# Kernel tuning notes

Hardware: AMD Instinct MI355X
Metric: run time of the kernel (lower is better)

The kernel has to match this reference:

```python
import jax, jax.numpy as jnp
import numpy as np

D_MODEL = 1024
D_HIDDEN = 4096
N_LATENTS = 64
D_LATENT = 1024
N_HEADS = 16
N_EXPERTS = 8
TOP_K = 2
B, T = 2, 2048
D_H = D_LATENT // N_HEADS  # 64


def setup_inputs() -> dict:
    key = jax.random.key(0)
    ks = jax.random.split(key, 16)
    x = jax.random.normal(ks[0], (B, T, D_MODEL), jnp.float32)
    # real RoPE cache (matches RoPE.build_rope_cache)
    half = D_H // 2
    inv_freq = 1.0 / (10000.0 ** (jnp.arange(half, dtype=jnp.float32) / half))
    ang = jnp.arange(T, dtype=jnp.float32)[:, None] * inv_freq[None, :]
    cos, sin = jnp.cos(ang), jnp.sin(ang)
    sL = D_LATENT ** -0.5
    sM = D_MODEL ** -0.5
    sH = D_HIDDEN ** -0.5
    def nrm(k, shape, sc):
        return jax.random.normal(k, shape, jnp.float32) * sc
    aks = jax.random.split(ks[1], 8)
    eks = jax.random.split(ks[2], 3)
    return {
        'x': x, 'cos': cos, 'sin': sin,
        'ln1_g': jnp.ones((D_MODEL,), jnp.float32), 'ln1_b': jnp.zeros((D_MODEL,), jnp.float32),
        'ln2_g': jnp.ones((D_MODEL,), jnp.float32), 'ln2_b': jnp.zeros((D_MODEL,), jnp.float32),
        'ln3_g': jnp.ones((D_MODEL,), jnp.float32), 'ln3_b': jnp.zeros((D_MODEL,), jnp.float32),
        'Lat': nrm(aks[0], (N_LATENTS, D_LATENT), sL),
        'Wq_lat': nrm(aks[1], (D_LATENT, D_LATENT), sL),
        'Wk_in': nrm(aks[2], (D_MODEL, D_LATENT), sM),
        'Wv_in': nrm(aks[3], (D_MODEL, D_LATENT), sM),
        'Wq_in': nrm(aks[4], (D_MODEL, D_LATENT), sM),
        'Wk_lat': nrm(aks[5], (D_LATENT, D_LATENT), sL),
        'Wv_lat': nrm(aks[6], (D_LATENT, D_LATENT), sL),
        'Wout_attn': nrm(aks[7], (D_LATENT, D_MODEL), sL),
        'router_W': nrm(ks[3], (D_MODEL, N_EXPERTS), sM),
        'router_b': jnp.zeros((N_EXPERTS,), jnp.float32),
        'expert_W': nrm(eks[0], (N_EXPERTS, D_MODEL, D_HIDDEN), sM),
        'expert_V': nrm(eks[1], (N_EXPERTS, D_MODEL, D_HIDDEN), sM),
        'expert_Wo': nrm(eks[2], (N_EXPERTS, D_HIDDEN, D_MODEL), sH),
        'lin_W': nrm(ks[4], (D_MODEL, D_MODEL), sM),
        'lin_b': jnp.zeros((D_MODEL,), jnp.float32),
    }


def _layernorm(x, g, b):
    mean = jnp.mean(x, axis=-1, keepdims=True)
    std = jnp.std(x, axis=-1, keepdims=True, ddof=1)  # torch std is unbiased
    return g * (x - mean) / (std + 1e-06) + b


def _split_heads(x):
    b, t, _ = x.shape
    return x.reshape(b, t, N_HEADS, D_H).transpose(0, 2, 1, 3)  # [b,h,t,dh]


def _merge_heads(x):
    b, h, t, dh = x.shape
    return x.transpose(0, 2, 1, 3).reshape(b, t, h * dh)


def _apply_rope(x, cos, sin):
    b, h, s, d = x.shape
    xr = x.reshape(b, h, s, d // 2, 2)
    x1, x2 = xr[..., 0], xr[..., 1]
    c = cos[:s][None, None]
    sn = sin[:s][None, None]
    o1 = x1 * c - x2 * sn
    o2 = x1 * sn + x2 * c
    return jnp.stack([o1, o2], axis=-1).reshape(b, h, s, d)


def _attn(Q, K, V):
    scores = jnp.einsum('bhqd,bhkd->bhqk', Q, K) / (D_H ** 0.5)
    w = jax.nn.softmax(scores, axis=-1)
    return jnp.einsum('bhqk,bhkd->bhqd', w, V)


def _mlha(x, cos, sin, Lat, Wq_lat, Wk_in, Wv_in, Wq_in, Wk_lat, Wv_lat, Wout_attn):
    b = x.shape[0]
    Lb = jnp.broadcast_to(Lat[None], (b, N_LATENTS, D_LATENT))
    Q = _split_heads(Lb @ Wq_lat)
    K = _apply_rope(_split_heads(x @ Wk_in), cos, sin)
    V = _split_heads(x @ Wv_in)
    z = _merge_heads(_attn(Q, K, V))              # [b, n_latents, d_latent]
    Ql = _split_heads(z @ Wq_lat)
    Kl = _split_heads(z @ Wk_lat)
    Vl = _split_heads(z @ Wv_lat)
    z2 = _merge_heads(_attn(Ql, Kl, Vl))          # [b, n_latents, d_latent]
    Qx = _apply_rope(_split_heads(x @ Wq_in), cos, sin)
    Kz = _split_heads(z2 @ Wk_lat)
    Vz = _split_heads(z2 @ Wv_lat)
    xl = _merge_heads(_attn(Qx, Kz, Vz))          # [b, T, d_latent]
    return xl @ Wout_attn


def _moe(x, router_W, router_b, expert_W, expert_V, expert_Wo):
    b, t, d = x.shape
    xf = x.reshape(b * t, d)
    logits = xf @ router_W + router_b                       # [N, E]
    topv, topi = jax.lax.top_k(logits, TOP_K)               # [N, k]
    probs = jax.nn.softmax(topv, axis=-1)                   # [N, k]
    out = jnp.zeros_like(xf)
    for e in range(N_EXPERTS):
        gate = jnp.sum(jnp.where(topi == e, probs, 0.0), axis=-1)  # [N]
        a = xf @ expert_W[e]
        bb = xf @ expert_V[e]
        y = (a * (bb * jax.nn.sigmoid(bb))) @ expert_Wo[e]
        out = out + gate[:, None] * y
    return out.reshape(b, t, d)


def reference(x, cos, sin, ln1_g, ln1_b, ln2_g, ln2_b, ln3_g, ln3_b,
              Lat, Wq_lat, Wk_in, Wv_in, Wq_in, Wk_lat, Wv_lat, Wout_attn,
              router_W, router_b, expert_W, expert_V, expert_Wo, lin_W, lin_b):
    attn = _mlha(x, cos, sin, Lat, Wq_lat, Wk_in, Wv_in, Wq_in, Wk_lat, Wv_lat, Wout_attn)
    x = _layernorm(x, ln1_g, ln1_b) + attn
    x = _layernorm(x, ln2_g, ln2_b) + _moe(x, router_W, router_b, expert_W, expert_V, expert_Wo)
    x = _layernorm(x, ln3_g, ln3_b) + (x @ lin_W + lin_b)
    return x
```

## Files before the change

### kernel.cpp

```cpp
#include <hip/hip_runtime.h>
#include <hip/hip_bf16.h>
#include <math.h>

typedef __hip_bfloat16 bf16;
typedef __attribute__((ext_vector_type(8))) short short8;
typedef __attribute__((ext_vector_type(8))) unsigned short ushort8;
typedef __attribute__((ext_vector_type(4))) float f32x4;

#define NT_   2048
#define NTOK_ 4096
#define DM_   1024
#define DHID_ 4096
#define NEXP_ 8

__device__ __forceinline__ unsigned short f2bf(float f) {
    unsigned u = __float_as_uint(f);
    u = u + 0x7FFF + ((u >> 16) & 1);
    return (unsigned short)(u >> 16);
}

__global__ __launch_bounds__(256) void c2b(const float* __restrict__ in,
        unsigned short* __restrict__ out, int n8)
{
    int i = blockIdx.x * 256 + threadIdx.x;
    if (i >= n8) return;
    const float4 v0 = *(const float4*)(in + (size_t)i * 8);
    const float4 v1 = *(const float4*)(in + (size_t)i * 8 + 4);
    ushort8 o;
    o[0] = f2bf(v0.x); o[1] = f2bf(v0.y); o[2] = f2bf(v0.z); o[3] = f2bf(v0.w);
    o[4] = f2bf(v1.x); o[5] = f2bf(v1.y); o[6] = f2bf(v1.z); o[7] = f2bf(v1.w);
    *(ushort8*)(out + (size_t)i * 8) = o;
}

__global__ __launch_bounds__(256) void tconv(const float* __restrict__ in,
        unsigned short* __restrict__ out, int R, int C)
{
    __shared__ float t[64][65];
    const size_t mofs = (size_t)blockIdx.z * R * C;
    const int r0 = blockIdx.y * 64, c0 = blockIdx.x * 64;
    const int tid = threadIdx.x;
    const int lr = tid >> 4, lc4 = (tid & 15) * 4;
    #pragma unroll
    for (int i = 0; i < 4; ++i) {
        float4 v = *(const float4*)(in + mofs + (size_t)(r0 + lr + i * 16) * C + c0 + lc4);
        t[lr + i * 16][lc4 + 0] = v.x; t[lr + i * 16][lc4 + 1] = v.y;
        t[lr + i * 16][lc4 + 2] = v.z; t[lr + i * 16][lc4 + 3] = v.w;
    }
    __syncthreads();
    const int oc = tid >> 2;
    const int j0 = (tid & 3) * 16;
    ushort8 o0, o1;
    #pragma unroll
    for (int j = 0; j < 8; ++j)  o0[j] = f2bf(t[j0 + j][oc]);
    #pragma unroll
    for (int j = 0; j < 8; ++j)  o1[j] = f2bf(t[j0 + 8 + j][oc]);
    size_t ob = mofs + (size_t)(c0 + oc) * R + r0 + j0;
    *(ushort8*)(out + ob) = o0;
    *(ushort8*)(out + ob + 8) = o1;
}

__global__ __launch_bounds__(256) void tconv3(const float* __restrict__ s0,
        const float* __restrict__ s1, const float* __restrict__ s2,
        unsigned short* __restrict__ out)
{
    __shared__ float t[64][65];
    const float* in = blockIdx.z == 0 ? s0 : (blockIdx.z == 1 ? s1 : s2);
    unsigned short* o = out + (size_t)blockIdx.z * DM_ * DM_;
    const int r0 = blockIdx.y * 64, c0 = blockIdx.x * 64;
    const int tid = threadIdx.x;
    const int lr = tid >> 4, lc4 = (tid & 15) * 4;
    #pragma unroll
    for (int i = 0; i < 4; ++i) {
        float4 v = *(const float4*)(in + (size_t)(r0 + lr + i * 16) * DM_ + c0 + lc4);
        t[lr + i * 16][lc4 + 0] = v.x; t[lr + i * 16][lc4 + 1] = v.y;
        t[lr + i * 16][lc4 + 2] = v.z; t[lr + i * 16][lc4 + 3] = v.w;
    }
    __syncthreads();
    const int oc = tid >> 2;
    const int j0 = (tid & 3) * 16;
    ushort8 o0, o1;
    #pragma unroll
    for (int j = 0; j < 8; ++j)  o0[j] = f2bf(t[j0 + j][oc]);
    #pragma unroll
    for (int j = 0; j < 8; ++j)  o1[j] = f2bf(t[j0 + 8 + j][oc]);
    size_t ob = (size_t)(c0 + oc) * DM_ + r0 + j0;
    *(ushort8*)(o + ob) = o0;
    *(ushort8*)(o + ob + 8) = o1;
}

__global__ __launch_bounds__(256) void gemm_bf16_128(
        const unsigned short* __restrict__ A, const unsigned short* __restrict__ BT,
        float* __restrict__ C, int M, int N, int K)
{
    __shared__ unsigned short As[128 * 64];
    __shared__ unsigned short Bs[128 * 64];
    const int tid = threadIdx.x;
    const int wid = tid >> 6, lane = tid & 63;
    const int m0 = blockIdx.y * 128, n0 = blockIdx.x * 128;

    const unsigned short* aSrc[4]; const unsigned short* bSrc[4]; int sWr[4];
    #pragma unroll
    for (int i = 0; i < 4; ++i) {
        int idx = tid + 256 * i;
        int row = idx >> 3, c8 = idx & 7;
        int ar = m0 + row; if (ar >= M) ar = M - 1;
        aSrc[i] = A + (size_t)ar * K + c8 * 8;
        bSrc[i] = BT + (size_t)(n0 + row) * K + c8 * 8;
        sWr[i] = (row * 128 + c8 * 16) ^ ((row & 7) << 4);
    }
    const int wr = wid >> 1, wc = wid & 1;
    int ra[2][4], rb[2][4];
    #pragma unroll
    for (int kk = 0; kk < 2; ++kk) {
        #pragma unroll
        for (int t = 0; t < 4; ++t) {
            int kb = kk * 64 + (lane >> 4) * 16;
            int rowa = wr * 64 + t * 16 + (lane & 15);
            ra[kk][t] = (rowa * 128 + kb) ^ ((rowa & 7) << 4);
            int rowb = wc * 64 + t * 16 + (lane & 15);
            rb[kk][t] = (rowb * 128 + kb) ^ ((rowb & 7) << 4);
        }
    }
    const f32x4 zero = {0.f, 0.f, 0.f, 0.f};
    f32x4 acc[4][4];
    #pragma unroll
    for (int i = 0; i < 4; ++i)
        #pragma unroll
        for (int j = 0; j < 4; ++j) acc[i][j] = zero;

    short8 sa[4], sb[4];
    #pragma unroll
    for (int i = 0; i < 4; ++i) { sa[i] = *(const short8*)(aSrc[i]); sb[i] = *(const short8*)(bSrc[i]); }
    const int nk = K >> 6;
    for (int kt = 0; kt < nk; ++kt) {
        #pragma unroll
        for (int i = 0; i < 4; ++i) {
            *(short8*)((char*)As + sWr[i]) = sa[i];
            *(short8*)((char*)Bs + sWr[i]) = sb[i];
        }
        __syncthreads();
        if (kt + 1 < nk) {
            int ko = (kt + 1) << 6;
            #pragma unroll
            for (int i = 0; i < 4; ++i) { sa[i] = *(const short8*)(aSrc[i] + ko); sb[i] = *(const short8*)(bSrc[i] + ko); }
        }
        #pragma unroll
        for (int kk = 0; kk < 2; ++kk) {
            short8 af[4], bfr[4];
            #pragma unroll
            for (int t = 0; t < 4; ++t) {
                af[t]  = *(const short8*)((const char*)As + ra[kk][t]);
                bfr[t] = *(const short8*)((const char*)Bs + rb[kk][t]);
            }
            #pragma unroll
            for (int i = 0; i < 4; ++i)
                #pragma unroll
                for (int j = 0; j < 4; ++j)
                    acc[i][j] = __builtin_amdgcn_mfma_f32_16x16x32_bf16(af[i], bfr[j], acc[i][j], 0, 0, 0);
        }
        __syncthreads();
    }
    const int cl = lane & 15, g4 = lane >> 4;
    #pragma unroll
    for (int i = 0; i < 4; ++i)
        #pragma unroll
        for (int j = 0; j < 4; ++j)
            #pragma unroll
            for (int r = 0; r < 4; ++r) {
                int rr = m0 + wr * 64 + i * 16 + g4 * 4 + r;
                if (rr < M) C[(size_t)rr * N + n0 + wc * 64 + j * 16 + cl] = acc[i][j][r];
            }
}

__global__ __launch_bounds__(256) void gemm_proj3(
        const unsigned short* __restrict__ A, const unsigned short* __restrict__ BT0,
        float* __restrict__ C0, const float* __restrict__ cosb,
        const float* __restrict__ sinb)
{
    const int z = blockIdx.z;
    const unsigned short* BT = BT0 + (size_t)z * DM_ * DM_;
    float* C = C0 + (size_t)z * NTOK_ * DM_;
    const bool doRope = (z != 1);
    __shared__ unsigned short As[128 * 64];
    __shared__ unsigned short Bs[128 * 64];
    const int tid = threadIdx.x;
    const int wid = tid >> 6, lane = tid & 63;
    const int m0 = blockIdx.y * 128, n0 = blockIdx.x * 128;
    const int K = DM_, N = DM_;

    const unsigned short* aSrc[4]; const unsigned short* bSrc[4]; int sWr[4];
    #pragma unroll
    for (int i = 0; i < 4; ++i) {
        int idx = tid + 256 * i;
        int row = idx >> 3, c8 = idx & 7;
        aSrc[i] = A + (size_t)(m0 + row) * K + c8 * 8;
        bSrc[i] = BT + (size_t)(n0 + row) * K + c8 * 8;
        sWr[i] = (row * 128 + c8 * 16) ^ ((row & 7) << 4);
    }
    const int wr = wid >> 1, wc = wid & 1;
    int ra[2][4], rb[2][4];
    #pragma unroll
    for (int kk = 0; kk < 2; ++kk) {
        #pragma unroll
        for (int t = 0; t < 4; ++t) {
            int kb = kk * 64 + (lane >> 4) * 16;
            int rowa = wr * 64 + t * 16 + (lane & 15);
            ra[kk][t] = (rowa * 128 + kb) ^ ((rowa & 7) << 4);
            int rowb = wc * 64 + t * 16 + (lane & 15);
            rb[kk][t] = (rowb * 128 + kb) ^ ((rowb & 7) << 4);
        }
    }
    const f32x4 zero = {0.f, 0.f, 0.f, 0.f};
    f32x4 acc[4][4];
    #pragma unroll
    for (int i = 0; i < 4; ++i)
        #pragma unroll
        for (int j = 0; j < 4; ++j) acc[i][j] = zero;

    short8 sa[4], sb[4];
    #pragma unroll
    for (int i = 0; i < 4; ++i) { sa[i] = *(const short8*)(aSrc[i]); sb[i] = *(const short8*)(bSrc[i]); }
    const int nk = K >> 6;
    for (int kt = 0; kt < nk; ++kt) {
        #pragma unroll
        for (int i = 0; i < 4; ++i) {
            *(short8*)((char*)As + sWr[i]) = sa[i];
            *(short8*)((char*)Bs + sWr[i]) = sb[i];
        }
        __syncthreads();
        if (kt + 1 < nk) {
            int ko = (kt + 1) << 6;
            #pragma unroll
            for (int i = 0; i < 4; ++i) { sa[i] = *(const short8*)(aSrc[i] + ko); sb[i] = *(const short8*)(bSrc[i] + ko); }
        }
        #pragma unroll
        for (int kk = 0; kk < 2; ++kk) {
            short8 af[4], bfr[4];
            #pragma unroll
            for (int t = 0; t < 4; ++t) {
                af[t]  = *(const short8*)((const char*)As + ra[kk][t]);
                bfr[t] = *(const short8*)((const char*)Bs + rb[kk][t]);
            }
            #pragma unroll
            for (int i = 0; i < 4; ++i)
                #pragma unroll
                for (int j = 0; j < 4; ++j)
                    acc[i][j] = __builtin_amdgcn_mfma_f32_16x16x32_bf16(af[i], bfr[j], acc[i][j], 0, 0, 0);
        }
        __syncthreads();
    }
    const int cl = lane & 15, g4 = lane >> 4;
    #pragma unroll
    for (int i = 0; i < 4; ++i)
        #pragma unroll
        for (int j = 0; j < 4; ++j) {
            const int cc = n0 + wc * 64 + j * 16 + cl;
            const int ii = (cc & 63) >> 1;
            const bool even = (cc & 1) == 0;
            #pragma unroll
            for (int r = 0; r < 4; ++r) {
                const int rr = m0 + wr * 64 + i * 16 + g4 * 4 + r;
                float v = acc[i][j][r];
                float p = __shfl_xor(v, 1, 64);
                float o = v;
                if (doRope) {
                    const int t = rr & (NT_ - 1);
                    float cv = cosb[t * 32 + ii], sv = sinb[t * 32 + ii];
                    o = even ? (v * cv - p * sv) : (p * sv + v * cv);
                }
                C[(size_t)rr * N + cc] = o;
            }
        }
}

__global__ __launch_bounds__(256) void gemm_lat(
        const unsigned short* __restrict__ A, const unsigned short* __restrict__ BT0,
        int btStride, float* __restrict__ C0, int cStride, int M)
{
    const int z = blockIdx.y;
    const unsigned short* BT = BT0 + (size_t)z * btStride;
    float* C = C0 + (size_t)z * cStride;
    const int n0 = blockIdx.x * 64;
    __shared__ unsigned short As[128 * 64];
    __shared__ unsigned short Bs[64 * 64];
    const int tid = threadIdx.x;
    const int wid = tid >> 6, lane = tid & 63;

    const unsigned short* aSrc[4]; int aWr[4];
    #pragma unroll
    for (int i = 0; i < 4; ++i) {
        int idx = tid + 256 * i;
        int row = idx >> 3, c8 = idx & 7;
        int ar = row; if (ar >= M) ar = M - 1;
        aSrc[i] = A + (size_t)ar * DM_ + c8 * 8;
        aWr[i] = (row * 128 + c8 * 16) ^ ((row & 7) << 4);
    }
    const unsigned short* bSrc[2]; int bWr[2];
    #pragma unroll
    for (int i = 0; i < 2; ++i) {
        int idx = tid + 256 * i;
        int row = idx >> 3, c8 = idx & 7;
        bSrc[i] = BT + (size_t)(n0 + row) * DM_ + c8 * 8;
        bWr[i] = (row * 128 + c8 * 16) ^ ((row & 7) << 4);
    }
    const int wr = wid >> 1, wc = wid & 1;
    int ra[2][4], rb[2][2];
    #pragma unroll
    for (int kk = 0; kk < 2; ++kk) {
        #pragma unroll
        for (int t = 0; t < 4; ++t) {
            int rowa = wr * 64 + t * 16 + (lane & 15);
            int kb = kk * 64 + (lane >> 4) * 16;
            ra[kk][t] = (rowa * 128 + kb) ^ ((rowa & 7) << 4);
        }
        #pragma unroll
        for (int t = 0; t < 2; ++t) {
            int rowb = wc * 32 + t * 16 + (lane & 15);
            int kb = kk * 64 + (lane >> 4) * 16;
            rb[kk][t] = (rowb * 128 + kb) ^ ((rowb & 7) << 4);
        }
    }
    const f32x4 zero = {0.f, 0.f, 0.f, 0.f};
    f32x4 acc[4][2];
    #pragma unroll
    for (int i = 0; i < 4; ++i)
        #pragma unroll
        for (int j = 0; j < 2; ++j) acc[i][j] = zero;

    short8 sa[4], sb[2];
    #pragma unroll
    for (int i = 0; i < 4; ++i) sa[i] = *(const short8*)(aSrc[i]);
    #pragma unroll
    for (int i = 0; i < 2; ++i) sb[i] = *(const short8*)(bSrc[i]);
    const int nk = DM_ >> 6;
    for (int kt = 0; kt < nk; ++kt) {
        #pragma unroll
        for (int i = 0; i < 4; ++i) *(short8*)((char*)As + aWr[i]) = sa[i];
        #pragma unroll
        for (int i = 0; i < 2; ++i) *(short8*)((char*)Bs + bWr[i]) = sb[i];
        __syncthreads();
        if (kt + 1 < nk) {
            int ko = (kt + 1) << 6;
            #pragma unroll
            for (int i = 0; i < 4; ++i) sa[i] = *(const short8*)(aSrc[i] + ko);
            #pragma unroll
            for (int i = 0; i < 2; ++i) sb[i] = *(const short8*)(bSrc[i] + ko);
        }
        #pragma unroll
        for (int kk = 0; kk < 2; ++kk) {
            short8 af[4], bf2[2];
            #pragma unroll
            for (int t = 0; t < 4; ++t) af[t] = *(const short8*)((const char*)As + ra[kk][t]);
            #pragma unroll
            for (int t = 0; t < 2; ++t) bf2[t] = *(const short8*)((const char*)Bs + rb[kk][t]);
            #pragma unroll
            for (int i = 0; i < 4; ++i)
                #pragma unroll
                for (int j = 0; j < 2; ++j)
                    acc[i][j] = __builtin_amdgcn_mfma_f32_16x16x32_bf16(af[i], bf2[j], acc[i][j], 0, 0, 0);
        }
        __syncthreads();
    }
    const int cl = lane & 15, g4 = lane >> 4;
    #pragma unroll
    for (int i = 0; i < 4; ++i)
        #pragma unroll
        for (int j = 0; j < 2; ++j)
            #pragma unroll
            for (int r = 0; r < 4; ++r) {
                int rl = wr * 64 + i * 16 + g4 * 4 + r;
                if (rl < M)
                    C[(size_t)rl * DM_ + n0 + wc * 32 + j * 16 + cl] = acc[i][j][r];
            }
}

__global__ __launch_bounds__(256) void attn_scores(float* __restrict__ S,
        const float* __restrict__ Q, const float* __restrict__ Km,
        int M, int T, int q_bs, int k_bs, float scale)
{
    const int bh = blockIdx.z, b = bh >> 4, h = bh & 15;
    const int t0 = blockIdx.x * 64, q0 = blockIdx.y * 64;
    __shared__ float Qs[64][65], Ks[64][65];
    const int tid = threadIdx.x;
    const int lr = tid >> 2, lc = (tid & 3) * 16;
    {
        int q = q0 + lr;
        if (q < M) {
            const float* Qp = Q + ((size_t)q_bs * b + q) * DM_ + h * 64 + lc;
            #pragma unroll
            for (int j = 0; j < 16; ++j) Qs[lr][lc + j] = Qp[j];
        } else {
            #pragma unroll
            for (int j = 0; j < 16; ++j) Qs[lr][lc + j] = 0.f;
        }
        const float* Kp = Km + ((size_t)k_bs * b + t0 + lr) * DM_ + h * 64 + lc;
        #pragma unroll
        for (int j = 0; j < 16; ++j) Ks[lr][lc + j] = Kp[j];
    }
    __syncthreads();
    const int ty = tid >> 4, tx = tid & 15;
    float acc[4][4] = {};
    for (int d = 0; d < 64; ++d) {
        float a[4], kk[4];
        #pragma unroll
        for (int i = 0; i < 4; ++i) a[i] = Qs[ty * 4 + i][d];
        #pragma unroll
        for (int j = 0; j < 4; ++j) kk[j] = Ks[tx * 4 + j][d];
        #pragma unroll
        for (int i = 0; i < 4; ++i)
            #pragma unroll
            for (int j = 0; j < 4; ++j) acc[i][j] += a[i] * kk[j];
    }
    #pragma unroll
    for (int i = 0; i < 4; ++i) {
        int q = q0 + ty * 4 + i;
        if (q < M) {
            float* Sp = S + ((size_t)bh * M + q) * T + t0 + tx * 4;
            #pragma unroll
            for (int j = 0; j < 4; ++j) Sp[j] = acc[i][j] * scale;
        }
    }
}

__global__ __launch_bounds__(256) void softmax_rows(float* __restrict__ S, int L)
{
    float* p = S + (size_t)blockIdx.x * L;
    const int tid = threadIdx.x;
    __shared__ float red[256];
    float m = -1e30f;
    for (int i = tid; i < L; i += 256) m = fmaxf(m, p[i]);
    red[tid] = m; __syncthreads();
    for (int s = 128; s; s >>= 1) { if (tid < s) red[tid] = fmaxf(red[tid], red[tid + s]); __syncthreads(); }
    m = red[0]; __syncthreads();
    float sum = 0.f;
    for (int i = tid; i < L; i += 256) { float e = __expf(p[i] - m); p[i] = e; sum += e; }
    red[tid] = sum; __syncthreads();
    for (int s = 128; s; s >>= 1) { if (tid < s) red[tid] += red[tid + s]; __syncthreads(); }
    float inv = 1.f / red[0];
    for (int i = tid; i < L; i += 256) p[i] *= inv;
}

__global__ __launch_bounds__(256) void softmax64(float* __restrict__ S)
{
    const int row = blockIdx.x * 4 + (threadIdx.x >> 6);
    const int lane = threadIdx.x & 63;
    float* p = S + (size_t)row * 64;
    float v = p[lane];
    float m = v;
    #pragma unroll
    for (int o = 32; o; o >>= 1) m = fmaxf(m, __shfl_xor(m, o, 64));
    float e = __expf(v - m);
    float s = e;
    #pragma unroll
    for (int o = 32; o; o >>= 1) s += __shfl_xor(s, o, 64);
    p[lane] = e / s;
}

__global__ __launch_bounds__(256) void pv_split(float* __restrict__ part,
        const float* __restrict__ P, const float* __restrict__ V)
{
    const int c = blockIdx.x, bh = blockIdx.y, b = bh >> 4, h = bh & 15;
    __shared__ float Ps[64][65], Vs[64][65];
    const int tid = threadIdx.x;
    const int lr = tid >> 2, lc = (tid & 3) * 16;
    const int ty = tid >> 4, tx = tid & 15;
    float acc[4][4] = {};
    for (int it = 0; it < 4; ++it) {
        const int t0 = c * 256 + it * 64;
        const float* Pp = P + ((size_t)bh * 64 + lr) * NT_ + t0 + lc;
        #pragma unroll
        for (int j = 0; j < 16; ++j) Ps[lr][lc + j] = Pp[j];
        const float* Vp = V + ((size_t)NT_ * b + t0 + lr) * DM_ + h * 64 + lc;
        #pragma unroll
        for (int j = 0; j < 16; ++j) Vs[lr][lc + j] = Vp[j];
        __syncthreads();
        for (int t = 0; t < 64; ++t) {
            float pp[4], vv[4];
            #pragma unroll
            for (int i = 0; i < 4; ++i) pp[i] = Ps[ty * 4 + i][t];
            #pragma unroll
            for (int j = 0; j < 4; ++j) vv[j] = Vs[t][tx * 4 + j];
            #pragma unroll
            for (int i = 0; i < 4; ++i)
                #pragma unroll
                for (int j = 0; j < 4; ++j) acc[i][j] += pp[i] * vv[j];
        }
        __syncthreads();
    }
    float* op = part + ((size_t)bh * 8 + c) * 4096;
    #pragma unroll
    for (int i = 0; i < 4; ++i)
        #pragma unroll
        for (int j = 0; j < 4; ++j)
            op[(ty * 4 + i) * 64 + tx * 4 + j] = acc[i][j];
}

__global__ __launch_bounds__(256) void pv_combine(const float* __restrict__ part,
        unsigned short* __restrict__ Zb)
{
    const int bh = blockIdx.x, b = bh >> 4, h = bh & 15;
    for (int idx = threadIdx.x; idx < 4096; idx += 256) {
        int q = idx >> 6, d = idx & 63;
        float s = 0.f;
        #pragma unroll
        for (int c = 0; c < 8; ++c) s += part[((size_t)bh * 8 + c) * 4096 + idx];
        Zb[(size_t)(b * 64 + q) * DM_ + h * 64 + d] = f2bf(s);
    }
}

__global__ __launch_bounds__(256) void attn_pv(float* __restrict__ Z,
        unsigned short* __restrict__ Zb,
        const float* __restrict__ P, const float* __restrict__ V,
        int M, int T, int v_bs)
{
    const int bh = blockIdx.y, b = bh >> 4, h = bh & 15;
    const int q0 = blockIdx.x * 64;
    __shared__ float Ps[64][65], Vs[64][65];
    const int tid = threadIdx.x;
    const int lr = tid >> 2, lc = (tid & 3) * 16;
    const int ty = tid >> 4, tx = tid & 15;
    float acc[4][4] = {};
    for (int t0 = 0; t0 < T; t0 += 64) {
        int q = q0 + lr;
        if (q < M) {
            const float* Pp = P + ((size_t)bh * M + q) * T + t0 + lc;
            #pragma unroll
            for (int j = 0; j < 16; ++j) Ps[lr][lc + j] = Pp[j];
        } else {
            #pragma unroll
            for (int j = 0; j < 16; ++j) Ps[lr][lc + j] = 0.f;
        }
        const float* Vp = V + ((size_t)v_bs * b + t0 + lr) * DM_ + h * 64 + lc;
        #pragma unroll
        for (int j = 0; j < 16; ++j) Vs[lr][lc + j] = Vp[j];
        __syncthreads();
        for (int t = 0; t < 64; ++t) {
            float pp[4], vv[4];
            #pragma unroll
            for (int i = 0; i < 4; ++i) pp[i] = Ps[ty * 4 + i][t];
            #pragma unroll
            for (int j = 0; j < 4; ++j) vv[j] = Vs[t][tx * 4 + j];
            #pragma unroll
            for (int i = 0; i < 4; ++i)
                #pragma unroll
                for (int j = 0; j < 4; ++j) acc[i][j] += pp[i] * vv[j];
        }
        __syncthreads();
    }
    #pragma unroll
    for (int i = 0; i < 4; ++i) {
        int q = q0 + ty * 4 + i;
        if (q < M) {
            size_t ofs = ((size_t)b * M + q) * DM_ + h * 64 + tx * 4;
            #pragma unroll
            for (int j = 0; j < 4; ++j) {
                Z[ofs + j] = acc[i][j];
                Zb[ofs + j] = f2bf(acc[i][j]);
            }
        }
    }
}

__global__ __launch_bounds__(256) void ln_add_dual(const float* __restrict__ X,
        const float* __restrict__ g, const float* __restrict__ bb,
        const float* __restrict__ add, float* __restrict__ out,
        unsigned short* __restrict__ outb)
{
    const int n = blockIdx.x, tid = threadIdx.x;
    const float* x = X + (size_t)n * DM_;
    __shared__ float red[256];
    float v[4]; float s = 0.f;
    #pragma unroll
    for (int i = 0; i < 4; ++i) { v[i] = x[tid + i * 256]; s += v[i]; }
    red[tid] = s; __syncthreads();
    for (int st = 128; st; st >>= 1) { if (tid < st) red[tid] += red[tid + st]; __syncthreads(); }
    float mean = red[0] * (1.f / 1024.f);
    __syncthreads();
    float vs = 0.f;
    #pragma unroll
    for (int i = 0; i < 4; ++i) { float d = v[i] - mean; vs += d * d; }
    red[tid] = vs; __syncthreads();
    for (int st = 128; st; st >>= 1) { if (tid < st) red[tid] += red[tid + st]; __syncthreads(); }
    float inv = 1.f / (sqrtf(red[0] * (1.f / 1023.f)) + 1e-6f);
    #pragma unroll
    for (int i = 0; i < 4; ++i) {
        int d = tid + i * 256;
        float r = g[d] * (v[i] - mean) * inv + bb[d] + add[(size_t)n * DM_ + d];
        out[(size_t)n * DM_ + d] = r;
        outb[(size_t)n * DM_ + d] = f2bf(r);
    }
}

__global__ __launch_bounds__(256) void ln_final(const float* __restrict__ X,
        const float* __restrict__ g, const float* __restrict__ bb,
        const float* __restrict__ t, const float* __restrict__ lb,
        float* __restrict__ out)
{
    const int n = blockIdx.x, tid = threadIdx.x;
    const float* x = X + (size_t)n * DM_;
    __shared__ float red[256];
    float v[4]; float s = 0.f;
    #pragma unroll
    for (int i = 0; i < 4; ++i) { v[i] = x[tid + i * 256]; s += v[i]; }
    red[tid] = s; __syncthreads();
    for (int st = 128; st; st >>= 1) { if (tid < st) red[tid] += red[tid + st]; __syncthreads(); }
    float mean = red[0] * (1.f / 1024.f);
    __syncthreads();
    float vs = 0.f;
    #pragma unroll
    for (int i = 0; i < 4; ++i) { float d = v[i] - mean; vs += d * d; }
    red[tid] = vs; __syncthreads();
    for (int st = 128; st; st >>= 1) { if (tid < st) red[tid] += red[tid + st]; __syncthreads(); }
    float inv = 1.f / (sqrtf(red[0] * (1.f / 1023.f)) + 1e-6f);
    #pragma unroll
    for (int i = 0; i < 4; ++i) {
        int d = tid + i * 256;
        out[(size_t)n * DM_ + d] = g[d] * (v[i] - mean) * inv + bb[d]
                                 + t[(size_t)n * DM_ + d] + lb[d];
    }
}

__global__ __launch_bounds__(256) void router_kernel(const float* __restrict__ X1,
        const float* __restrict__ Wr, const float* __restrict__ br,
        int* __restrict__ topi, float* __restrict__ gates, int* __restrict__ counts)
{
    const int n = blockIdx.x, tid = threadIdx.x;
    const int e = tid >> 5, l = tid & 31;
    const float* x = X1 + (size_t)n * DM_;
    float s = 0.f;
    for (int k = l; k < DM_; k += 32) s += x[k] * Wr[k * NEXP_ + e];
    for (int off = 16; off; off >>= 1) s += __shfl_down(s, off, 32);
    __shared__ float lg[NEXP_];
    if (l == 0) lg[e] = s + br[e];
    __syncthreads();
    if (tid == 0) {
        float v1 = -1e30f; int i1 = 0;
        for (int ee = 0; ee < NEXP_; ++ee) if (lg[ee] > v1) { v1 = lg[ee]; i1 = ee; }
        float v2 = -1e30f; int i2 = 0;
        for (int ee = 0; ee < NEXP_; ++ee) if (ee != i1 && lg[ee] > v2) { v2 = lg[ee]; i2 = ee; }
        float e2 = __expf(v2 - v1);
        float inv = 1.f / (1.f + e2);
        topi[n * 2] = i1; topi[n * 2 + 1] = i2;
        gates[n * 2] = inv; gates[n * 2 + 1] = e2 * inv;
        atomicAdd(&counts[i1], 1); atomicAdd(&counts[i2], 1);
    }
}

__global__ void zero_counts(int* __restrict__ counts)
{
    if (threadIdx.x < NEXP_) counts[threadIdx.x] = 0;
}

__global__ void router_offsets(const int* __restrict__ counts, int* __restrict__ offs,
                               int* __restrict__ fill)
{
    if (threadIdx.x == 0) {
        int acc = 0;
        for (int e = 0; e < NEXP_; ++e) { offs[e] = acc; acc += counts[e]; fill[e] = 0; }
    }
}

__global__ __launch_bounds__(256) void router_scatter(const int* __restrict__ topi,
        int* __restrict__ fill, const int* __restrict__ offs,
        int* __restrict__ ptok, int* __restrict__ pidx)
{
    int n = blockIdx.x * 256 + threadIdx.x;
    if (n >= NTOK_) return;
    #pragma unroll
    for (int s2 = 0; s2 < 2; ++s2) {
        int e = topi[n * 2 + s2];
        int r = atomicAdd(&fill[e], 1);
        int p = offs[e] + r;
        ptok[p] = n;
        pidx[n * 2 + s2] = p;
    }
}

__global__ __launch_bounds__(256) void moe_up_mfma(
        const unsigned short* __restrict__ X1b,
        const unsigned short* __restrict__ WTa, const unsigned short* __restrict__ VTa,
        unsigned short* __restrict__ H,
        const int* __restrict__ cnt, const int* __restrict__ offs,
        const int* __restrict__ ptok)
{
    const int e = blockIdx.z;
    const int ce = cnt[e];
    const int m0 = blockIdx.y * 128;
    if (m0 >= ce) return;
    const int n0 = blockIdx.x * 64;
    const int base = offs[e];
    const unsigned short* WT = WTa + (size_t)e * DHID_ * DM_;
    const unsigned short* VT = VTa + (size_t)e * DHID_ * DM_;
    __shared__ unsigned short As[128 * 64];
    __shared__ unsigned short Ws[64 * 64];
    __shared__ unsigned short Vs[64 * 64];
    __shared__ int rtok[128];
    const int tid = threadIdx.x;
    const int wid = tid >> 6, lane = tid & 63;
    if (tid < 128) {
        int r = m0 + tid;
        rtok[tid] = (r < ce) ? ptok[base + r] : ptok[base + ce - 1];
    }
    __syncthreads();

    const unsigned short* aSrc[4]; int aWr[4];
    #pragma unroll
    for (int i = 0; i < 4; ++i) {
        int idx = tid + 256 * i;
        int row = idx >> 3, c8 = idx & 7;
        aSrc[i] = X1b + (size_t)rtok[row] * DM_ + c8 * 8;
        aWr[i] = (row * 128 + c8 * 16) ^ ((row & 7) << 4);
    }
    const unsigned short* wSrc[2]; const unsigned short* vSrc[2]; int bWr[2];
    #pragma unroll
    for (int i = 0; i < 2; ++i) {
        int idx = tid + 256 * i;
        int row = idx >> 3, c8 = idx & 7;
        wSrc[i] = WT + (size_t)(n0 + row) * DM_ + c8 * 8;
        vSrc[i] = VT + (size_t)(n0 + row) * DM_ + c8 * 8;
        bWr[i] = (row * 128 + c8 * 16) ^ ((row & 7) << 4);
    }
    const int wr = wid >> 1, wc = wid & 1;
    int ra[2][4], rb[2][2];
    #pragma unroll
    for (int kk = 0; kk < 2; ++kk) {
        #pragma unroll
        for (int t = 0; t < 4; ++t) {
            int rowa = wr * 64 + t * 16 + (lane & 15);
            int kb = kk * 64 + (lane >> 4) * 16;
            ra[kk][t] = (rowa * 128 + kb) ^ ((rowa & 7) << 4);
        }
        #pragma unroll
        for (int t = 0; t < 2; ++t) {
            int rowb = wc * 32 + t * 16 + (lane & 15);
            int kb = kk * 64 + (lane >> 4) * 16;
            rb[kk][t] = (rowb * 128 + kb) ^ ((rowb & 7) << 4);
        }
    }
    const f32x4 zero = {0.f, 0.f, 0.f, 0.f};
    f32x4 accw[4][2], accv[4][2];
    #pragma unroll
    for (int i = 0; i < 4; ++i)
        #pragma unroll
        for (int j = 0; j < 2; ++j) { accw[i][j] = zero; accv[i][j] = zero; }

    short8 sa[4], sw[2], sv[2];
    #pragma unroll
    for (int i = 0; i < 4; ++i) sa[i] = *(const short8*)(aSrc[i]);
    #pragma unroll
    for (int i = 0; i < 2; ++i) { sw[i] = *(const short8*)(wSrc[i]); sv[i] = *(const short8*)(vSrc[i]); }
    const int nk = DM_ >> 6;
    for (int kt = 0; kt < nk; ++kt) {
        #pragma unroll
        for (int i = 0; i < 4; ++i) *(short8*)((char*)As + aWr[i]) = sa[i];
        #pragma unroll
        for (int i = 0; i < 2; ++i) {
            *(short8*)((char*)Ws + bWr[i]) = sw[i];
            *(short8*)((char*)Vs + bWr[i]) = sv[i];
        }
        __syncthreads();
        if (kt + 1 < nk) {
            int ko = (kt + 1) << 6;
            #pragma unroll
            for (int i = 0; i < 4; ++i) sa[i] = *(const short8*)(aSrc[i] + ko);
            #pragma unroll
            for (int i = 0; i < 2; ++i) { sw[i] = *(const short8*)(wSrc[i] + ko); sv[i] = *(const short8*)(vSrc[i] + ko); }
        }
        #pragma unroll
        for (int kk = 0; kk < 2; ++kk) {
            short8 af[4], bw[2], bv[2];
            #pragma unroll
            for (int t = 0; t < 4; ++t) af[t] = *(const short8*)((const char*)As + ra[kk][t]);
            #pragma unroll
            for (int t = 0; t < 2; ++t) {
                bw[t] = *(const short8*)((const char*)Ws + rb[kk][t]);
                bv[t] = *(const short8*)((const char*)Vs + rb[kk][t]);
            }
            #pragma unroll
            for (int i = 0; i < 4; ++i)
                #pragma unroll
                for (int j = 0; j < 2; ++j) {
                    accw[i][j] = __builtin_amdgcn_mfma_f32_16x16x32_bf16(af[i], bw[j], accw[i][j], 0, 0, 0);
                    accv[i][j] = __builtin_amdgcn_mfma_f32_16x16x32_bf16(af[i], bv[j], accv[i][j], 0, 0, 0);
                }
        }
        __syncthreads();
    }
    const int cl = lane & 15, g4 = lane >> 4;
    #pragma unroll
    for (int i = 0; i < 4; ++i)
        #pragma unroll
        for (int j = 0; j < 2; ++j)
            #pragma unroll
            for (int r = 0; r < 4; ++r) {
                int rl = m0 + wr * 64 + i * 16 + g4 * 4 + r;
                if (rl < ce) {
                    float a = accw[i][j][r], b = accv[i][j][r];
                    float h = a * (b / (1.f + __expf(-b)));
                    H[(size_t)(base + rl) * DHID_ + n0 + wc * 32 + j * 16 + cl] = f2bf(h);
                }
            }
}

__global__ __launch_bounds__(256) void moe_down_mfma(
        const unsigned short* __restrict__ H, const unsigned short* __restrict__ WoTa,
        float* __restrict__ PY,
        const int* __restrict__ cnt, const int* __restrict__ offs)
{
    const int e = blockIdx.z;
    const int ce = cnt[e];
    const int m0 = blockIdx.y * 128;
    if (m0 >= ce) return;
    const int n0 = blockIdx.x * 128;
    const int base = offs[e];
    const unsigned short* WoT = WoTa + (size_t)e * DM_ * DHID_;
    __shared__ unsigned short As[128 * 64];
    __shared__ unsigned short Bs[128 * 64];
    const int tid = threadIdx.x;
    const int wid = tid >> 6, lane = tid & 63;

    const unsigned short* aSrc[4]; const unsigned short* bSrc[4]; int sWr[4];
    #pragma unroll
    for (int i = 0; i < 4; ++i) {
        int idx = tid + 256 * i;
        int row = idx >> 3, c8 = idx & 7;
        int r = m0 + row; if (r >= ce) r = ce - 1;
        aSrc[i] = H + (size_t)(base + r) * DHID_ + c8 * 8;
        bSrc[i] = WoT + (size_t)(n0 + row) * DHID_ + c8 * 8;
        sWr[i] = (row * 128 + c8 * 16) ^ ((row & 7) << 4);
    }
    const int wr = wid >> 1, wc = wid & 1;
    int ra[2][4], rb[2][4];
    #pragma unroll
    for (int kk = 0; kk < 2; ++kk) {
        #pragma unroll
        for (int t = 0; t < 4; ++t) {
            int kb = kk * 64 + (lane >> 4) * 16;
            int rowa = wr * 64 + t * 16 + (lane & 15);
            ra[kk][t] = (rowa * 128 + kb) ^ ((rowa & 7) << 4);
            int rowb = wc * 64 + t * 16 + (lane & 15);
            rb[kk][t] = (rowb * 128 + kb) ^ ((rowb & 7) << 4);
        }
    }
    const f32x4 zero = {0.f, 0.f, 0.f, 0.f};
    f32x4 acc[4][4];
    #pragma unroll
    for (int i = 0; i < 4; ++i)
        #pragma unroll
        for (int j = 0; j < 4; ++j) acc[i][j] = zero;

    short8 sa[4], sb[4];
    #pragma unroll
    for (int i = 0; i < 4; ++i) { sa[i] = *(const short8*)(aSrc[i]); sb[i] = *(const short8*)(bSrc[i]); }
    const int nk = DHID_ >> 6;
    for (int kt = 0; kt < nk; ++kt) {
        #pragma unroll
        for (int i = 0; i < 4; ++i) {
            *(short8*)((char*)As + sWr[i]) = sa[i];
            *(short8*)((char*)Bs + sWr[i]) = sb[i];
        }
        __syncthreads();
        if (kt + 1 < nk) {
            int ko = (kt + 1) << 6;
            #pragma unroll
            for (int i = 0; i < 4; ++i) { sa[i] = *(const short8*)(aSrc[i] + ko); sb[i] = *(const short8*)(bSrc[i] + ko); }
        }
        #pragma unroll
        for (int kk = 0; kk < 2; ++kk) {
            short8 af[4], bfr[4];
            #pragma unroll
            for (int t = 0; t < 4; ++t) {
                af[t]  = *(const short8*)((const char*)As + ra[kk][t]);
                bfr[t] = *(const short8*)((const char*)Bs + rb[kk][t]);
            }
            #pragma unroll
            for (int i = 0; i < 4; ++i)
                #pragma unroll
                for (int j = 0; j < 4; ++j)
                    acc[i][j] = __builtin_amdgcn_mfma_f32_16x16x32_bf16(af[i], bfr[j], acc[i][j], 0, 0, 0);
        }
        __syncthreads();
    }
    const int cl = lane & 15, g4 = lane >> 4;
    #pragma unroll
    for (int i = 0; i < 4; ++i)
        #pragma unroll
        for (int j = 0; j < 4; ++j)
            #pragma unroll
            for (int r = 0; r < 4; ++r) {
                int rl = m0 + wr * 64 + i * 16 + g4 * 4 + r;
                if (rl < ce)
                    PY[(size_t)(base + rl) * DM_ + n0 + wc * 64 + j * 16 + cl] = acc[i][j][r];
            }
}

__global__ __launch_bounds__(256) void moe_combine(const float* __restrict__ PY,
        const int* __restrict__ pidx, const float* __restrict__ gates,
        float* __restrict__ MO)
{
    int n = blockIdx.x, tid = threadIdx.x;
    int p0 = pidx[n * 2], p1 = pidx[n * 2 + 1];
    float g0 = gates[n * 2], g1 = gates[n * 2 + 1];
    #pragma unroll
    for (int i = 0; i < 4; ++i) {
        int d = tid + i * 256;
        MO[(size_t)n * DM_ + d] = g0 * PY[(size_t)p0 * DM_ + d] + g1 * PY[(size_t)p1 * DM_ + d];
    }
}

extern "C" void kernel_launch(void* const* d_in, const int* in_sizes, int n_in,
                              void* d_out, int out_size, void* d_ws, size_t ws_size,
                              hipStream_t stream)
{
    const float* x      = (const float*)d_in[0];
    const float* cosb   = (const float*)d_in[1];
    const float* sinb   = (const float*)d_in[2];
    const float* ln1g   = (const float*)d_in[3];
    const float* ln1b   = (const float*)d_in[4];
    const float* ln2g   = (const float*)d_in[5];
    const float* ln2b   = (const float*)d_in[6];
    const float* ln3g   = (const float*)d_in[7];
    const float* ln3b   = (const float*)d_in[8];
    const float* Lat    = (const float*)d_in[9];
    const float* Wq_lat = (const float*)d_in[10];
    const float* Wk_in  = (const float*)d_in[11];
    const float* Wv_in  = (const float*)d_in[12];
    const float* Wq_in  = (const float*)d_in[13];
    const float* Wk_lat = (const float*)d_in[14];
    const float* Wv_lat = (const float*)d_in[15];
    const float* Wout   = (const float*)d_in[16];
    const float* rW     = (const float*)d_in[17];
    const float* rb     = (const float*)d_in[18];
    const float* eW     = (const float*)d_in[19];
    const float* eV     = (const float*)d_in[20];
    const float* eWo    = (const float*)d_in[21];
    const float* linW   = (const float*)d_in[22];
    const float* linb   = (const float*)d_in[23];
    float* out = (float*)d_out;

    float* ws = (float*)d_ws;
    const size_t M1 = 1024 * 1024;
    float* buf0 = ws;
    float* buf1 = ws + 4 * M1;
    float* buf2 = ws + 8 * M1;
    float* buf3 = ws + 12 * M1;
    size_t off = 16 * M1;
    float* qlat = ws + off; off += 65536;
    float* qlb  = ws + off; off += 131072;
    float* klb  = ws + off; off += 131072;
    float* vlb  = ws + off; off += 131072;
    float* s2b  = ws + off; off += 131072;
    float* z2b  = ws + off; off += 131072;
    float* kzb  = ws + off; off += 131072;
    float* vzb  = ws + off; off += 131072;
    float* gates = ws + off; off += 8192;
    int* iarea = (int*)(ws + off); off += 32768;
    int* topi   = iarea;
    int* counts = iarea + 8192;
    int* offs   = iarea + 8200;
    int* fill   = iarea + 8208;
    int* ptok   = iarea + 8216;
    int* pidx   = iarea + 16408;
    unsigned short* zb_b  = (unsigned short*)(ws + off); off += 65536;
    unsigned short* z2b_b = (unsigned short*)(ws + off); off += 65536;
    unsigned short* latb  = (unsigned short*)(ws + off); off += 32768;
    unsigned short* x1b   = (unsigned short*)(ws + off); off += 2 * M1;
    unsigned short* WkT   = (unsigned short*)(ws + off); off += 3 * (M1 / 2);
    unsigned short* WoutT = (unsigned short*)(ws + off); off += M1 / 2;
    unsigned short* linWT = (unsigned short*)(ws + off); off += M1 / 2;
    unsigned short* WlatT = (unsigned short*)(ws + off); off += 3 * (M1 / 2);

    unsigned short* Hbuf  = (unsigned short*)(ws + 24 * M1);
    unsigned short* actb  = (unsigned short*)(ws + 24 * M1);
    unsigned short* x2b   = (unsigned short*)(ws + 24 * M1);
    float* pvpart         = ws + 26 * M1;
    unsigned short* eWT   = (unsigned short*)(ws + 40 * M1);
    unsigned short* eVT   = (unsigned short*)(ws + 56 * M1);
    unsigned short* eWoT  = eWT;
    float* PY             = ws + 56 * M1;

    dim3 blk(256);

    zero_counts<<<1, 64, 0, stream>>>(counts);

    tconv3<<<dim3(16, 16, 3), blk, 0, stream>>>(Wk_in, Wv_in, Wq_in, WkT);
    tconv<<<dim3(16, 16, 1), blk, 0, stream>>>(Wout, WoutT, 1024, 1024);
    tconv<<<dim3(16, 16, 1), blk, 0, stream>>>(linW, linWT, 1024, 1024);
    tconv3<<<dim3(16, 16, 3), blk, 0, stream>>>(Wq_lat, Wk_lat, Wv_lat, WlatT);
    tconv<<<dim3(64, 16, 8), blk, 0, stream>>>(eW, eWT, 1024, 4096);
    tconv<<<dim3(64, 16, 8), blk, 0, stream>>>(eV, eVT, 1024, 4096);
    c2b<<<2048, blk, 0, stream>>>(x, actb, 524288);
    c2b<<<32, blk, 0, stream>>>(Lat, latb, 8192);

    gemm_lat<<<dim3(16, 1), blk, 0, stream>>>(latb, WlatT, (int)M1, qlat, 0, 64);

    gemm_proj3<<<dim3(8, 32, 3), blk, 0, stream>>>(actb, WkT, buf0, cosb, sinb);

    attn_scores<<<dim3(32, 1, 32), blk, 0, stream>>>(buf3, qlat, buf0, 64, 2048, 0, 2048, 0.125f);
    softmax_rows<<<2048, blk, 0, stream>>>(buf3, 2048);
    pv_split<<<dim3(8, 32), blk, 0, stream>>>(pvpart, buf3, buf1);
    pv_combine<<<32, blk, 0, stream>>>(pvpart, zb_b);

    gemm_lat<<<dim3(16, 3), blk, 0, stream>>>(zb_b, WlatT, (int)M1, qlb, 131072, 128);
    attn_scores<<<dim3(1, 1, 32), blk, 0, stream>>>(s2b, qlb, klb, 64, 64, 64, 64, 0.125f);
    softmax64<<<512, blk, 0, stream>>>(s2b);
    attn_pv<<<dim3(1, 32), blk, 0, stream>>>(z2b, z2b_b, s2b, vlb, 64, 64, 64);

    gemm_lat<<<dim3(16, 2), blk, 0, stream>>>(z2b_b, WlatT + M1, (int)M1, kzb, 131072, 128);
    attn_scores<<<dim3(1, 32, 32), blk, 0, stream>>>(buf3, buf2, kzb, 2048, 64, 2048, 64, 0.125f);
    softmax64<<<16384, blk, 0, stream>>>(buf3);
    attn_pv<<<dim3(32, 32), blk, 0, stream>>>(buf0, actb, buf3, vzb, 2048, 64, 64);
    gemm_bf16_128<<<dim3(8, 32), blk, 0, stream>>>(actb, WoutT, buf1, 4096, 1024, 1024);

    ln_add_dual<<<4096, blk, 0, stream>>>(x, ln1g, ln1b, buf1, buf2, x1b);

    router_kernel<<<4096, blk, 0, stream>>>(buf2, rW, rb, topi, gates, counts);
    router_offsets<<<1, 64, 0, stream>>>(counts, offs, fill);
    router_scatter<<<16, blk, 0, stream>>>(topi, fill, offs, ptok, pidx);
    moe_up_mfma<<<dim3(64, 32, 8), blk, 0, stream>>>(x1b, eWT, eVT, Hbuf, counts, offs, ptok);
    tconv<<<dim3(16, 64, 8), blk, 0, stream>>>(eWo, eWoT, 4096, 1024);
    moe_down_mfma<<<dim3(8, 32, 8), blk, 0, stream>>>(Hbuf, eWoT, PY, counts, offs);
    moe_combine<<<4096, blk, 0, stream>>>(PY, pidx, gates, buf0);

    ln_add_dual<<<4096, blk, 0, stream>>>(buf2, ln2g, ln2b, buf0, buf1, x2b);

    gemm_bf16_128<<<dim3(8, 32), blk, 0, stream>>>(x2b, linWT, buf3, 4096, 1024, 1024);
    ln_final<<<4096, blk, 0, stream>>>(buf1, ln3g, ln3b, buf3, linb, out);
}
```

Baseline: 1.022 ms.

## Fuse 64-key attention scores, softmax and PV into one kernel

Replaces the three-kernel sequence (attn_scores, softmax64, attn_pv) for the two attention stages with 64 keys with a single fused kernel. The kernel keeps Q, K and V tiles in shared memory, computes scores, applies softmax with in-register shuffles and multiplies by V without writing the score matrix to global memory. This removes the round trip of a 4096x64 fp32 score matrix per head and two kernel launches per stage. It also drops the fp32 Z output and writes only bf16, and it uses about 50KB of shared memory per block, which may limit occupancy.

```diff
diff --git a/kernel.cpp b/kernel.cpp
--- a/kernel.cpp
+++ b/kernel.cpp
@@ -440,20 +440,81 @@
     for (int i = tid; i < L; i += 256) p[i] *= inv;
 }
 
-__global__ __launch_bounds__(256) void softmax64(float* __restrict__ S)
-{
-    const int row = blockIdx.x * 4 + (threadIdx.x >> 6);
-    const int lane = threadIdx.x & 63;
-    float* p = S + (size_t)row * 64;
-    float v = p[lane];
-    float m = v;
-    #pragma unroll
-    for (int o = 32; o; o >>= 1) m = fmaxf(m, __shfl_xor(m, o, 64));
-    float e = __expf(v - m);
-    float s = e;
-    #pragma unroll
-    for (int o = 32; o; o >>= 1) s += __shfl_xor(s, o, 64);
-    p[lane] = e / s;
+__global__ __launch_bounds__(256) void fused_attn64(unsigned short* __restrict__ Ob,
+        const float* __restrict__ Q, const float* __restrict__ Kp,
+        const float* __restrict__ Vp, int q_bs)
+{
+    const int bh = blockIdx.y, b = bh >> 4, h = bh & 15;
+    const int q0 = blockIdx.x * 64;
+    __shared__ float Qs[64][65], Ks[64][65], Vs[64][65];
+    __shared__ float ls[64];
+    const int tid = threadIdx.x;
+    const int lr = tid >> 2, lc = (tid & 3) * 16;
+    {
+        const float* Qr = Q + ((size_t)q_bs * b + q0 + lr) * DM_ + h * 64 + lc;
+        #pragma unroll
+        for (int j = 0; j < 16; ++j) Qs[lr][lc + j] = Qr[j];
+        const float* Kr = Kp + ((size_t)64 * b + lr) * DM_ + h * 64 + lc;
+        #pragma unroll
+        for (int j = 0; j < 16; ++j) Ks[lr][lc + j] = Kr[j];
+        const float* Vr = Vp + ((size_t)64 * b + lr) * DM_ + h * 64 + lc;
+        #pragma unroll
+        for (int j = 0; j < 16; ++j) Vs[lr][lc + j] = Vr[j];
+    }
+    __syncthreads();
+    const int ty = tid >> 4, tx = tid & 15;
+    float acc[4][4] = {};
+    for (int d = 0; d < 64; ++d) {
+        float a[4], kk[4];
+        #pragma unroll
+        for (int i = 0; i < 4; ++i) a[i] = Qs[ty * 4 + i][d];
+        #pragma unroll
+        for (int j = 0; j < 4; ++j) kk[j] = Ks[tx * 4 + j][d];
+        #pragma unroll
+        for (int i = 0; i < 4; ++i)
+            #pragma unroll
+            for (int j = 0; j < 4; ++j) acc[i][j] += a[i] * kk[j];
+    }
+    float p[4][4]; float lsum[4];
+    #pragma unroll
+    for (int i = 0; i < 4; ++i) {
+        float m = fmaxf(fmaxf(acc[i][0], acc[i][1]), fmaxf(acc[i][2], acc[i][3]));
+        #pragma unroll
+        for (int o = 1; o <= 8; o <<= 1) m = fmaxf(m, __shfl_xor(m, o, 64));
+        float s = 0.f;
+        #pragma unroll
+        for (int j = 0; j < 4; ++j) { p[i][j] = __expf(acc[i][j] * 0.125f - m * 0.125f); s += p[i][j]; }
+        #pragma unroll
+        for (int o = 1; o <= 8; o <<= 1) s += __shfl_xor(s, o, 64);
+        lsum[i] = s;
+    }
+    __syncthreads();
+    #pragma unroll
+    for (int i = 0; i < 4; ++i) {
+        #pragma unroll
+        for (int j = 0; j < 4; ++j) Qs[ty * 4 + i][tx * 4 + j] = p[i][j];
+        if (tx == 0) ls[ty * 4 + i] = lsum[i];
+    }
+    __syncthreads();
+    float O[4][4] = {};
+    for (int t = 0; t < 64; ++t) {
+        float pp[4], vv[4];
+        #pragma unroll
+        for (int i = 0; i < 4; ++i) pp[i] = Qs[ty * 4 + i][t];
+        #pragma unroll
+        for (int j = 0; j < 4; ++j) vv[j] = Vs[t][tx * 4 + j];
+        #pragma unroll
+        for (int i = 0; i < 4; ++i)
+            #pragma unroll
+            for (int j = 0; j < 4; ++j) O[i][j] += pp[i] * vv[j];
+    }
+    #pragma unroll
+    for (int i = 0; i < 4; ++i) {
+        float inv = 1.f / ls[ty * 4 + i];
+        size_t ofs = ((size_t)q_bs * b + q0 + ty * 4 + i) * DM_ + h * 64 + tx * 4;
+        #pragma unroll
+        for (int j = 0; j < 4; ++j) Ob[ofs + j] = f2bf(O[i][j] * inv);
+    }
 }
 
 __global__ __launch_bounds__(256) void pv_split(float* __restrict__ part,
@@ -505,59 +566,6 @@
         #pragma unroll
         for (int c = 0; c < 8; ++c) s += part[((size_t)bh * 8 + c) * 4096 + idx];
         Zb[(size_t)(b * 64 + q) * DM_ + h * 64 + d] = f2bf(s);
-    }
-}
-
-__global__ __launch_bounds__(256) void attn_pv(float* __restrict__ Z,
-        unsigned short* __restrict__ Zb,
-        const float* __restrict__ P, const float* __restrict__ V,
-        int M, int T, int v_bs)
-{
-    const int bh = blockIdx.y, b = bh >> 4, h = bh & 15;
-    const int q0 = blockIdx.x * 64;
-    __shared__ float Ps[64][65], Vs[64][65];
-    const int tid = threadIdx.x;
-    const int lr = tid >> 2, lc = (tid & 3) * 16;
-    const int ty = tid >> 4, tx = tid & 15;
-    float acc[4][4] = {};
-    for (int t0 = 0; t0 < T; t0 += 64) {
-        int q = q0 + lr;
-        if (q < M) {
-            const float* Pp = P + ((size_t)bh * M + q) * T + t0 + lc;
-            #pragma unroll
-            for (int j = 0; j < 16; ++j) Ps[lr][lc + j] = Pp[j];
-        } else {
-            #pragma unroll
-            for (int j = 0; j < 16; ++j) Ps[lr][lc + j] = 0.f;
-        }
-        const float* Vp = V + ((size_t)v_bs * b + t0 + lr) * DM_ + h * 64 + lc;
-        #pragma unroll
-        for (int j = 0; j < 16; ++j) Vs[lr][lc + j] = Vp[j];
-        __syncthreads();
-        for (int t = 0; t < 64; ++t) {
-            float pp[4], vv[4];
-            #pragma unroll
-            for (int i = 0; i < 4; ++i) pp[i] = Ps[ty * 4 + i][t];
-            #pragma unroll
-            for (int j = 0; j < 4; ++j) vv[j] = Vs[t][tx * 4 + j];
-            #pragma unroll
-            for (int i = 0; i < 4; ++i)
-                #pragma unroll
-                for (int j = 0; j < 4; ++j) acc[i][j] += pp[i] * vv[j];
-        }
-        __syncthreads();
-    }
-    #pragma unroll
-    for (int i = 0; i < 4; ++i) {
-        int q = q0 + ty * 4 + i;
-        if (q < M) {
-            size_t ofs = ((size_t)b * M + q) * DM_ + h * 64 + tx * 4;
-            #pragma unroll
-            for (int j = 0; j < 4; ++j) {
-                Z[ofs + j] = acc[i][j];
-                Zb[ofs + j] = f2bf(acc[i][j]);
-            }
-        }
     }
 }
 
@@ -1002,14 +1010,10 @@
     pv_combine<<<32, blk, 0, stream>>>(pvpart, zb_b);
 
     gemm_lat<<<dim3(16, 3), blk, 0, stream>>>(zb_b, WlatT, (int)M1, qlb, 131072, 128);
-    attn_scores<<<dim3(1, 1, 32), blk, 0, stream>>>(s2b, qlb, klb, 64, 64, 64, 64, 0.125f);
-    softmax64<<<512, blk, 0, stream>>>(s2b);
-    attn_pv<<<dim3(1, 32), blk, 0, stream>>>(z2b, z2b_b, s2b, vlb, 64, 64, 64);
+    fused_attn64<<<dim3(1, 32), blk, 0, stream>>>(z2b_b, qlb, klb, vlb, 64);
 
     gemm_lat<<<dim3(16, 2), blk, 0, stream>>>(z2b_b, WlatT + M1, (int)M1, kzb, 131072, 128);
-    attn_scores<<<dim3(1, 32, 32), blk, 0, stream>>>(buf3, buf2, kzb, 2048, 64, 2048, 64, 0.125f);
-    softmax64<<<16384, blk, 0, stream>>>(buf3);
-    attn_pv<<<dim3(32, 32), blk, 0, stream>>>(buf0, actb, buf3, vzb, 2048, 64, 64);
+    fused_attn64<<<dim3(32, 32), blk, 0, stream>>>(actb, buf2, kzb, vzb, 2048);
     gemm_bf16_128<<<dim3(8, 32), blk, 0, stream>>>(actb, WoutT, buf1, 4096, 1024, 1024);
 
     ln_add_dual<<<4096, blk, 0, stream>>>(x, ln1g, ln1b, buf1, buf2, x1b);
```

New measurement: 997.9 us. -2.3%, faster.
